# Kernel tuning notes

Measured on AMD Instinct MI355X. Metric: run time of the kernel, lower is better.

Reference implementation:

```python
import jax, jax.numpy as jnp
import numpy as np

B, N, C, H, V = 32, 1024, 512, 256, 50  # batch, positions, post_conv_out_channels, hidden_size, out_channels


def setup_inputs() -> dict:
    key = jax.random.key(0)
    ks = jax.random.split(key, 9)
    s = 0.05
    p = lambda k, shape: jax.random.normal(k, shape, jnp.float32) * s
    return dict(
        features=jax.random.normal(ks[0], (B, N, C), jnp.float32),
        w_i2h=p(ks[1], (H, C)),              # input_to_hidden (no bias)
        w_h2h=p(ks[2], (H, H)), b_h2h=jnp.zeros((H,), jnp.float32),
        w_score=p(ks[3], (H,)),              # score Linear(H,1,no bias)
        w_gru_ih=p(ks[4], (3 * H, C + V)), w_gru_hh=p(ks[5], (3 * H, H)),
        b_gru_ih=jnp.zeros((3 * H,), jnp.float32), b_gru_hh=jnp.zeros((3 * H,), jnp.float32),
        w_s1=p(ks[6], (H, H)), b_s1=jnp.zeros((H,), jnp.float32),
        w_s2=p(ks[7], (V, H)), b_s2=jnp.zeros((V,), jnp.float32),
        max_text_length=500,
    )


def reference(features, w_i2h, w_h2h, b_h2h, w_score, w_gru_ih, w_gru_hh,
              b_gru_ih, b_gru_hh, w_s1, b_s1, w_s2, b_s2, max_text_length):
    batch = features.shape[0]
    hid = w_h2h.shape[0]
    vocab = w_s2.shape[0]
    steps = max_text_length + 1
    # input_to_hidden(features) is loop-invariant -> hoist out of the recurrence
    feat_proj = jnp.einsum('bnc,hc->bnh', features, w_i2h)

    def gru_cell(x, h):
        gi = x @ w_gru_ih.T + b_gru_ih
        gh = h @ w_gru_hh.T + b_gru_hh
        i_r, i_z, i_n = jnp.split(gi, 3, axis=-1)
        h_r, h_z, h_n = jnp.split(gh, 3, axis=-1)
        r = jax.nn.sigmoid(i_r + h_r)
        z = jax.nn.sigmoid(i_z + h_z)
        n = jnp.tanh(i_n + r * h_n)
        return (1.0 - z) * n + z * h

    def step(carry, _):
        h, pre = carry
        prev_proj = h @ w_h2h.T + b_h2h                      # [B,H]
        scores = jnp.tanh(feat_proj + prev_proj[:, None, :]) @ w_score  # [B,N]
        alpha = jax.nn.softmax(scores, axis=1)
        ctx = jnp.einsum('bn,bnc->bc', alpha, features)      # [B,C]
        onehot = jax.nn.one_hot(pre, vocab, dtype=features.dtype)
        h_new = gru_cell(jnp.concatenate([ctx, onehot], axis=-1), h)
        struct = (h_new @ w_s1.T + b_s1) @ w_s2.T + b_s2     # structure_generator, [B,V]
        pre_new = jnp.argmax(struct, axis=-1)
        return (h_new, pre_new), struct

    h0 = jnp.zeros((batch, hid), features.dtype)
    pre0 = jnp.zeros((batch,), jnp.int32)
    _, structs = jax.lax.scan(step, (h0, pre0), None, length=steps)  # [T,B,V]
    structs = jnp.transpose(structs, (1, 0, 2))                      # [B,T,V]
    return jax.nn.softmax(structs, axis=-1)
```

## Files before the change

kernel.cpp:

```cpp
#include <hip/hip_runtime.h>
#include <math.h>

#define B_ 32
#define N_ 1024
#define C_ 512
#define H_ 256
#define V_ 50
#define T_ 501
#define CV_ 562
#define G3_ 768
#define CHUNKS_ 32
#define POSB_ 32

typedef float    f32x4 __attribute__((ext_vector_type(4)));
typedef _Float16 f16x4 __attribute__((ext_vector_type(4)));
typedef _Float16 f16x8 __attribute__((ext_vector_type(8)));

__device__ __forceinline__ float fast_rcp(float x) { return __builtin_amdgcn_rcpf(x); }
__device__ __forceinline__ float fast_tanh(float x) {
  float e = __expf(2.0f * x);
  return 1.0f - 2.0f * fast_rcp(e + 1.0f);
}
__device__ __forceinline__ float fast_sigmoid(float x) {
  return fast_rcp(1.0f + __expf(-x));
}
__device__ __forceinline__ void astore(float* p, float v) {
  __hip_atomic_store(p, v, __ATOMIC_RELAXED, __HIP_MEMORY_SCOPE_AGENT);
}
__device__ __forceinline__ float aload(const float* p) {
  return __hip_atomic_load(p, __ATOMIC_RELAXED, __HIP_MEMORY_SCOPE_AGENT);
}
__device__ __forceinline__ int aloadi(const int* p) {
  return __hip_atomic_load(p, __ATOMIC_RELAXED, __HIP_MEMORY_SCOPE_AGENT);
}

__global__ __launch_bounds__(256) void fp_gemm(const float* __restrict__ A,
                                               const float* __restrict__ W,
                                               _Float16* __restrict__ FPh) {
  __shared__ __align__(16) float As[16][68];
  __shared__ __align__(16) float Ws[16][68];
  const int t = threadIdx.x;
  const int m0 = blockIdx.x * 64;
  const int h0 = blockIdx.y * 64;
  const int lr = t & 63;
  const int kg = t >> 6;
  const int tx = t & 15, ty = t >> 4;
  float acc[4][4] = {};
  for (int k0 = 0; k0 < C_; k0 += 16) {
    float4 av = *(const float4*)&A[(size_t)(m0 + lr) * C_ + k0 + kg * 4];
    float4 wv = *(const float4*)&W[(size_t)(h0 + lr) * C_ + k0 + kg * 4];
    As[kg*4+0][lr] = av.x; As[kg*4+1][lr] = av.y; As[kg*4+2][lr] = av.z; As[kg*4+3][lr] = av.w;
    Ws[kg*4+0][lr] = wv.x; Ws[kg*4+1][lr] = wv.y; Ws[kg*4+2][lr] = wv.z; Ws[kg*4+3][lr] = wv.w;
    __syncthreads();
#pragma unroll
    for (int kk = 0; kk < 16; ++kk) {
      float4 a = *(const float4*)&As[kk][ty * 4];
      float4 w = *(const float4*)&Ws[kk][tx * 4];
      acc[0][0] += a.x*w.x; acc[0][1] += a.x*w.y; acc[0][2] += a.x*w.z; acc[0][3] += a.x*w.w;
      acc[1][0] += a.y*w.x; acc[1][1] += a.y*w.y; acc[1][2] += a.y*w.z; acc[1][3] += a.y*w.w;
      acc[2][0] += a.z*w.x; acc[2][1] += a.z*w.y; acc[2][2] += a.z*w.z; acc[2][3] += a.z*w.w;
      acc[3][0] += a.w*w.x; acc[3][1] += a.w*w.y; acc[3][2] += a.w*w.z; acc[3][3] += a.w*w.w;
    }
    __syncthreads();
  }
#pragma unroll
  for (int i = 0; i < 4; ++i) {
    f16x4 o;
    o.x = (_Float16)acc[i][0]; o.y = (_Float16)acc[i][1];
    o.z = (_Float16)acc[i][2]; o.w = (_Float16)acc[i][3];
    *(f16x4*)&FPh[(size_t)(m0 + ty*4 + i) * H_ + h0 + tx*4] = o;
  }
}

__global__ void feat_to_fp16(const float* __restrict__ src, _Float16* __restrict__ dst,
                             int total4) {
  int i = blockIdx.x * 256 + threadIdx.x;
  if (i >= total4) return;
  f32x4 v = *(const f32x4*)&src[(size_t)i * 4];
  f16x4 o; o.x = (_Float16)v.x; o.y = (_Float16)v.y; o.z = (_Float16)v.z; o.w = (_Float16)v.w;
  *(f16x4*)&dst[(size_t)i * 4] = o;
}

__global__ void transpose_split(const float* __restrict__ src, float* __restrict__ dstA,
                                float* __restrict__ dstB, int rows, int cols, int splitc) {
  int i = blockIdx.x * 256 + threadIdx.x;
  if (i >= rows * cols) return;
  int j = i / cols, c = i - j * cols;
  float v = src[i];
  if (c < splitc) dstA[(size_t)c * rows + j] = v;
  else            dstB[(size_t)(c - splitc) * rows + j] = v;
}

__global__ void init_kernel(const float* __restrict__ b_h2h, float* __restrict__ h,
                            float* __restrict__ pp, int* __restrict__ pre,
                            int* __restrict__ cnt1, int* __restrict__ cnt2) {
  int i = blockIdx.x * blockDim.x + threadIdx.x;
  if (i < B_ * H_) { h[i] = 0.0f; pp[i] = b_h2h[i & (H_ - 1)]; }
  if (i < B_) pre[i] = 0;
  if (i < T_ * B_ * 16) cnt1[i] = 0;
  if (i < T_ * 16) cnt2[i] = 0;
}

__global__ __launch_bounds__(256) void k1_attn(
    int tstep,
    const _Float16* __restrict__ feath, const _Float16* __restrict__ fph,
    const float* __restrict__ w_score, const float* __restrict__ pp,
    float* __restrict__ part_ctx, float* __restrict__ part_l, int* __restrict__ cnt1,
    float* __restrict__ ctx_raw, float* __restrict__ l_total) {
  __shared__ __align__(16) float lds_ctx[4 * C_];
  __shared__ float lds_l[4];
  __shared__ int sflag;

  const int t = threadIdx.x;
  const int wv = t >> 6;
  const int lane = t & 63;
  const int b = blockIdx.x >> 5;
  const int chunk = blockIdx.x & (CHUNKS_ - 1);

  float4 ppr = *(const float4*)&pp[b * H_ + lane * 4];
  float4 wsr = *(const float4*)&w_score[lane * 4];
  float aA0 = 0.f, aA1 = 0.f, aA2 = 0.f, aA3 = 0.f;
  float aB0 = 0.f, aB1 = 0.f, aB2 = 0.f, aB3 = 0.f;
  float lacc = 0.f;
  const _Float16* fphb = fph + (size_t)b * N_ * H_;
  const _Float16* fbb  = feath + (size_t)b * N_ * C_;
  const int n0 = chunk * POSB_ + wv * 8;
#pragma unroll 2
  for (int i = 0; i < 8; ++i) {
    const int n = n0 + i;
    f16x4 v = __builtin_nontemporal_load((const f16x4*)&fphb[(size_t)n * H_ + lane * 4]);
    float s = fast_tanh((float)v.x + ppr.x) * wsr.x + fast_tanh((float)v.y + ppr.y) * wsr.y
            + fast_tanh((float)v.z + ppr.z) * wsr.z + fast_tanh((float)v.w + ppr.w) * wsr.w;
#pragma unroll
    for (int off = 32; off > 0; off >>= 1) s += __shfl_xor(s, off);
    float p = __expf(s);
    lacc += p;
    f16x8 f = __builtin_nontemporal_load((const f16x8*)&fbb[(size_t)n * C_ + lane * 8]);
    aA0 += p * (float)f.s0; aA1 += p * (float)f.s1; aA2 += p * (float)f.s2; aA3 += p * (float)f.s3;
    aB0 += p * (float)f.s4; aB1 += p * (float)f.s5; aB2 += p * (float)f.s6; aB3 += p * (float)f.s7;
  }
  {
    float4 o0; o0.x = aA0; o0.y = aA1; o0.z = aA2; o0.w = aA3;
    float4 o1; o1.x = aB0; o1.y = aB1; o1.z = aB2; o1.w = aB3;
    *(float4*)&lds_ctx[wv * C_ + lane * 8] = o0;
    *(float4*)&lds_ctx[wv * C_ + lane * 8 + 4] = o1;
  }
  if (lane == 0) lds_l[wv] = lacc;
  __syncthreads();
  {
    float c0 = lds_ctx[t] + lds_ctx[C_ + t] + lds_ctx[2 * C_ + t] + lds_ctx[3 * C_ + t];
    float c1 = lds_ctx[t + 256] + lds_ctx[C_ + t + 256] + lds_ctx[2 * C_ + t + 256] + lds_ctx[3 * C_ + t + 256];
    float* pc = &part_ctx[((size_t)b * CHUNKS_ + chunk) * C_];
    astore(&pc[t], c0);
    astore(&pc[t + 256], c1);
    if (t == 0) astore(&part_l[b * CHUNKS_ + chunk], lds_l[0] + lds_l[1] + lds_l[2] + lds_l[3]);
  }
  asm volatile("s_waitcnt vmcnt(0)" ::: "memory");
  __syncthreads();
  if (t == 0) sflag = atomicAdd(&cnt1[(tstep * B_ + b) * 16], 1);
  __syncthreads();
  if (sflag != CHUNKS_ - 1) return;

  float d0 = 0.f, d1 = 0.f;
  const float* src = part_ctx + (size_t)b * CHUNKS_ * C_;
#pragma unroll 8
  for (int ch = 0; ch < CHUNKS_; ++ch) {
    d0 += aload(&src[(size_t)ch * C_ + t]);
    d1 += aload(&src[(size_t)ch * C_ + t + 256]);
  }
  ctx_raw[b * C_ + t] = d0;
  ctx_raw[b * C_ + t + 256] = d1;
  if (t < 64) {
    float lv = (t < CHUNKS_) ? aload(&part_l[b * CHUNKS_ + t]) : 0.0f;
#pragma unroll
    for (int off = 32; off > 0; off >>= 1) lv += __shfl_xor(lv, off);
    if (t == 0) l_total[b] = lv;
  }
}

__global__ __launch_bounds__(256) void k2_fused(
    int tstep,
    const float* __restrict__ ctx_raw, float* __restrict__ h,
    const float* __restrict__ WtA, const float* __restrict__ WtH,
    float* __restrict__ pgi, float* __restrict__ pgh,
    const float* __restrict__ l_total,
    const float* __restrict__ WtO,
    const float* __restrict__ b_gru_ih, const float* __restrict__ b_gru_hh,
    const float* __restrict__ Wt_s1, const float* __restrict__ b_s1,
    const float* __restrict__ Wt_h2h, const float* __restrict__ b_h2h,
    const float* __restrict__ w_s2, const float* __restrict__ b_s2,
    float* __restrict__ pp, int* __restrict__ pre,
    int* __restrict__ cnt2, float* __restrict__ out) {
  __shared__ __align__(16) float smem[6144];
  __shared__ int sflag;
  const int t = threadIdx.x;
  const int j0 = (blockIdx.x % 12) * 64;
  const int ks = blockIdx.x / 12;
  float* wlds = smem;
  float* clds = smem + 4096;
  const int jl = (t & 31) * 2;
  const int b0 = (t >> 5) * 4;

  float acc[2][4] = {};
#pragma unroll
  for (int kt = 0; kt < 2; ++kt) {
    const int k0 = ks * 128 + kt * 64;
    __syncthreads();
#pragma unroll
    for (int q = 0; q < 4; ++q) {
      int idx = q * 256 + t; int r = idx >> 4, f4 = (idx & 15) * 4;
      *(float4*)&wlds[r * 64 + f4] = *(const float4*)&WtA[(size_t)(k0 + r) * G3_ + j0 + f4];
    }
#pragma unroll
    for (int q = 0; q < 2; ++q) {
      int idx = q * 256 + t; int bb = idx >> 4, f4 = (idx & 15) * 4;
      *(float4*)&clds[bb * 64 + f4] = *(const float4*)&ctx_raw[(size_t)bb * C_ + k0 + f4];
    }
    __syncthreads();
#pragma unroll 8
    for (int k = 0; k < 64; ++k) {
      float w0 = wlds[k * 64 + jl], w1 = wlds[k * 64 + jl + 1];
      float x0 = clds[b0 * 64 + k], x1 = clds[(b0 + 1) * 64 + k];
      float x2 = clds[(b0 + 2) * 64 + k], x3 = clds[(b0 + 3) * 64 + k];
      acc[0][0] += w0 * x0; acc[0][1] += w0 * x1; acc[0][2] += w0 * x2; acc[0][3] += w0 * x3;
      acc[1][0] += w1 * x0; acc[1][1] += w1 * x1; acc[1][2] += w1 * x2; acc[1][3] += w1 * x3;
    }
  }
#pragma unroll
  for (int i = 0; i < 2; ++i)
#pragma unroll
    for (int q = 0; q < 4; ++q)
      astore(&pgi[((size_t)ks * B_ + b0 + q) * G3_ + j0 + jl + i], acc[i][q]);

  float acb[2][4] = {};
  {
    const int k0 = ks * 64;
    __syncthreads();
#pragma unroll
    for (int q = 0; q < 4; ++q) {
      int idx = q * 256 + t; int r = idx >> 4, f4 = (idx & 15) * 4;
      *(float4*)&wlds[r * 64 + f4] = *(const float4*)&WtH[(size_t)(k0 + r) * G3_ + j0 + f4];
    }
#pragma unroll
    for (int q = 0; q < 2; ++q) {
      int idx = q * 256 + t; int bb = idx >> 4, f4 = (idx & 15) * 4;
      *(float4*)&clds[bb * 64 + f4] = *(const float4*)&h[(size_t)bb * H_ + k0 + f4];
    }
    __syncthreads();
#pragma unroll 8
    for (int k = 0; k < 64; ++k) {
      float w0 = wlds[k * 64 + jl], w1 = wlds[k * 64 + jl + 1];
      float x0 = clds[b0 * 64 + k], x1 = clds[(b0 + 1) * 64 + k];
      float x2 = clds[(b0 + 2) * 64 + k], x3 = clds[(b0 + 3) * 64 + k];
      acb[0][0] += w0 * x0; acb[0][1] += w0 * x1; acb[0][2] += w0 * x2; acb[0][3] += w0 * x3;
      acb[1][0] += w1 * x0; acb[1][1] += w1 * x1; acb[1][2] += w1 * x2; acb[1][3] += w1 * x3;
    }
  }
#pragma unroll
  for (int i = 0; i < 2; ++i)
#pragma unroll
    for (int q = 0; q < 4; ++q)
      astore(&pgh[((size_t)ks * B_ + b0 + q) * G3_ + j0 + jl + i], acb[i][q]);

  asm volatile("s_waitcnt vmcnt(0)" ::: "memory");
  __syncthreads();
  if (t == 0) sflag = atomicAdd(&cnt2[tstep * 16], 1);
  __syncthreads();
  const int ticket = sflag;
  if (ticket < 16) return;
  if (t == 0) {
    while (aloadi(&cnt2[tstep * 16]) < 48) __builtin_amdgcn_s_sleep(2);
  }
  __syncthreads();

  const int b = ticket - 16;
  float* shn = smem;
  float* ss1 = smem + 256;
  float* sst = smem + 512;
  const int prev = pre[b];
  const float invl = 1.0f / l_total[b];
  float gi0 = 0.f, gi1 = 0.f, gi2 = 0.f, gh0 = 0.f, gh1 = 0.f, gh2 = 0.f;
#pragma unroll
  for (int k = 0; k < 4; ++k) {
    const float* pg = pgi + ((size_t)k * B_ + b) * G3_;
    const float* ph = pgh + ((size_t)k * B_ + b) * G3_;
    gi0 += aload(&pg[t]); gi1 += aload(&pg[t + 256]); gi2 += aload(&pg[t + 512]);
    gh0 += aload(&ph[t]); gh1 += aload(&ph[t + 256]); gh2 += aload(&ph[t + 512]);
  }
  const float* wo = WtO + (size_t)prev * G3_;
  gi0 = gi0 * invl + b_gru_ih[t]       + wo[t];
  gi1 = gi1 * invl + b_gru_ih[t + 256] + wo[t + 256];
  gi2 = gi2 * invl + b_gru_ih[t + 512] + wo[t + 512];
  gh0 += b_gru_hh[t]; gh1 += b_gru_hh[t + 256]; gh2 += b_gru_hh[t + 512];
  const float h_old = h[b * H_ + t];
  const float r = fast_sigmoid(gi0 + gh0);
  const float z = fast_sigmoid(gi1 + gh1);
  const float nn = fast_tanh(gi2 + r * gh2);
  const float hnew = (1.0f - z) * nn + z * h_old;
  h[b * H_ + t] = hnew;
  shn[t] = hnew;
  __syncthreads();

  {
    float a1 = b_s1[t], a2 = b_h2h[t];
    const float* w1 = Wt_s1 + t;
    const float* w2 = Wt_h2h + t;
#pragma unroll 8
    for (int c = 0; c < H_; ++c) {
      float v = shn[c];
      a1 += w1[(size_t)c * H_] * v;
      a2 += w2[(size_t)c * H_] * v;
    }
    ss1[t] = a1;
    pp[b * H_ + t] = a2;
  }
  __syncthreads();

  const int wv = t >> 6, lane = t & 63;
  for (int v = wv; v < V_; v += 4) {
    float4 wr = *(const float4*)&w_s2[(size_t)v * H_ + lane * 4];
    float4 sv = *(const float4*)&ss1[lane * 4];
    float acc2 = wr.x * sv.x + wr.y * sv.y + wr.z * sv.z + wr.w * sv.w;
#pragma unroll
    for (int off = 32; off > 0; off >>= 1) acc2 += __shfl_xor(acc2, off);
    if (lane == 0) sst[v] = acc2 + b_s2[v];
  }
  __syncthreads();

  if (t < 64) {
    float val = (lane < V_) ? sst[lane] : -INFINITY;
    float m = val;
#pragma unroll
    for (int off = 32; off > 0; off >>= 1) m = fmaxf(m, __shfl_xor(m, off));
    unsigned long long msk = __ballot(val == m);
    int amax = __ffsll(msk) - 1;
    float e = (lane < V_) ? __expf(val - m) : 0.0f;
    float ssum = e;
#pragma unroll
    for (int off = 32; off > 0; off >>= 1) ssum += __shfl_xor(ssum, off);
    if (lane < V_) out[((size_t)b * T_ + tstep) * V_ + lane] = e / ssum;
    if (lane == 0) pre[b] = amax;
  }
}

extern "C" void kernel_launch(void* const* d_in, const int* in_sizes, int n_in,
                              void* d_out, int out_size, void* d_ws, size_t ws_size,
                              hipStream_t stream) {
  (void)in_sizes; (void)n_in; (void)out_size; (void)ws_size;
  const float* feat     = (const float*)d_in[0];
  const float* w_i2h    = (const float*)d_in[1];
  const float* w_h2h    = (const float*)d_in[2];
  const float* b_h2h    = (const float*)d_in[3];
  const float* w_score  = (const float*)d_in[4];
  const float* w_gru_ih = (const float*)d_in[5];
  const float* w_gru_hh = (const float*)d_in[6];
  const float* b_gru_ih = (const float*)d_in[7];
  const float* b_gru_hh = (const float*)d_in[8];
  const float* w_s1     = (const float*)d_in[9];
  const float* b_s1     = (const float*)d_in[10];
  const float* w_s2     = (const float*)d_in[11];
  const float* b_s2     = (const float*)d_in[12];
  float* out = (float*)d_out;

  char* ws = (char*)d_ws;
  size_t off = 0;
  auto alloc = [&](size_t bytes) { void* p = ws + off; off += (bytes + 255) & ~(size_t)255; return p; };
  _Float16* fph   = (_Float16*)alloc((size_t)B_ * N_ * H_ * 2);
  _Float16* feath = (_Float16*)alloc((size_t)B_ * N_ * C_ * 2);
  float* part_ctx = (float*)alloc((size_t)B_ * CHUNKS_ * C_ * 4);
  float* part_l   = (float*)alloc((size_t)B_ * CHUNKS_ * 4);
  float* ctx_raw  = (float*)alloc((size_t)B_ * C_ * 4);
  float* l_total  = (float*)alloc((size_t)B_ * 4);
  float* pgi      = (float*)alloc((size_t)4 * B_ * G3_ * 4);
  float* pgh      = (float*)alloc((size_t)4 * B_ * G3_ * 4);
  float* WtA      = (float*)alloc((size_t)C_ * G3_ * 4);
  float* WtO      = (float*)alloc((size_t)V_ * G3_ * 4);
  float* WtH      = (float*)alloc((size_t)H_ * G3_ * 4);
  float* Wt_s1    = (float*)alloc((size_t)H_ * H_ * 4);
  float* Wt_h2h   = (float*)alloc((size_t)H_ * H_ * 4);
  float* h        = (float*)alloc((size_t)B_ * H_ * 4);
  float* pp       = (float*)alloc((size_t)B_ * H_ * 4);
  int*   pre      = (int*)alloc((size_t)B_ * 4);
  int*   cnt1     = (int*)alloc((size_t)T_ * B_ * 16 * 4);
  int*   cnt2     = (int*)alloc((size_t)T_ * 16 * 4);

  init_kernel<<<(T_ * B_ * 16 + 255) / 256, 256, 0, stream>>>(b_h2h, h, pp, pre, cnt1, cnt2);
  fp_gemm<<<dim3((B_ * N_) / 64, H_ / 64), 256, 0, stream>>>(feat, w_i2h, fph);
  feat_to_fp16<<<(B_ * N_ * C_ / 4 + 255) / 256, 256, 0, stream>>>(feat, feath, B_ * N_ * C_ / 4);
  transpose_split<<<(G3_ * CV_ + 255) / 256, 256, 0, stream>>>(w_gru_ih, WtA, WtO, G3_, CV_, C_);
  transpose_split<<<(G3_ * H_ + 255) / 256, 256, 0, stream>>>(w_gru_hh, WtH, WtH, G3_, H_, H_);
  transpose_split<<<(H_ * H_ + 255) / 256, 256, 0, stream>>>(w_s1, Wt_s1, Wt_s1, H_, H_, H_);
  transpose_split<<<(H_ * H_ + 255) / 256, 256, 0, stream>>>(w_h2h, Wt_h2h, Wt_h2h, H_, H_, H_);

  for (int tstep = 0; tstep < T_; ++tstep) {
    k1_attn<<<B_ * CHUNKS_, 256, 0, stream>>>(tstep, feath, fph, w_score, pp,
                                              part_ctx, part_l, cnt1, ctx_raw, l_total);
    k2_fused<<<48, 256, 0, stream>>>(tstep, ctx_raw, h, WtA, WtH, pgi, pgh, l_total,
                                     WtO, b_gru_ih, b_gru_hh, Wt_s1, b_s1, Wt_h2h, b_h2h,
                                     w_s2, b_s2, pp, pre, cnt2, out);
  }
}
```

Measured before the change: 18.11 ms.

## Move chunk reduction from attention kernel into tail kernel with grid barriers

The attention kernel no longer does the last-block atomic ticket and the cross-chunk reduction. It just writes partial context sums, and it now issues all eight position loads up front so more memory requests are in flight. The tail kernel's first 32 blocks reduce the partials per batch, then all 48 blocks pass a spin barrier before the GRU gate GEMM. A second barrier replaces the ticket-based election of the 32 GRU finisher blocks. This shortens the attention kernel's critical path, at the cost of an extra grid-wide spin barrier inside the tail kernel and more registers in the attention kernel.

```diff
diff --git a/kernel.cpp b/kernel.cpp
--- a/kernel.cpp
+++ b/kernel.cpp
@@ -93,23 +93,19 @@
 
 __global__ void init_kernel(const float* __restrict__ b_h2h, float* __restrict__ h,
                             float* __restrict__ pp, int* __restrict__ pre,
-                            int* __restrict__ cnt1, int* __restrict__ cnt2) {
+                            int* __restrict__ cnt) {
   int i = blockIdx.x * blockDim.x + threadIdx.x;
   if (i < B_ * H_) { h[i] = 0.0f; pp[i] = b_h2h[i & (H_ - 1)]; }
   if (i < B_) pre[i] = 0;
-  if (i < T_ * B_ * 16) cnt1[i] = 0;
-  if (i < T_ * 16) cnt2[i] = 0;
+  if (i < T_ * 16) cnt[i] = 0;
 }
 
 __global__ __launch_bounds__(256) void k1_attn(
-    int tstep,
     const _Float16* __restrict__ feath, const _Float16* __restrict__ fph,
     const float* __restrict__ w_score, const float* __restrict__ pp,
-    float* __restrict__ part_ctx, float* __restrict__ part_l, int* __restrict__ cnt1,
-    float* __restrict__ ctx_raw, float* __restrict__ l_total) {
+    float* __restrict__ part_ctx, float* __restrict__ part_l) {
   __shared__ __align__(16) float lds_ctx[4 * C_];
   __shared__ float lds_l[4];
-  __shared__ int sflag;
 
   const int t = threadIdx.x;
   const int wv = t >> 6;
@@ -119,25 +115,31 @@
 
   float4 ppr = *(const float4*)&pp[b * H_ + lane * 4];
   float4 wsr = *(const float4*)&w_score[lane * 4];
+  const int n0 = chunk * POSB_ + wv * 8;
+  const _Float16* fp0 = fph + (size_t)b * N_ * H_ + (size_t)n0 * H_ + lane * 4;
+  const _Float16* ft0 = feath + (size_t)b * N_ * C_ + (size_t)n0 * C_ + lane * 8;
+
+  f16x4 v[8];
+  f16x8 f[8];
+#pragma unroll
+  for (int i = 0; i < 8; ++i) {
+    v[i] = __builtin_nontemporal_load((const f16x4*)(fp0 + (size_t)i * H_));
+    f[i] = __builtin_nontemporal_load((const f16x8*)(ft0 + (size_t)i * C_));
+  }
+
   float aA0 = 0.f, aA1 = 0.f, aA2 = 0.f, aA3 = 0.f;
   float aB0 = 0.f, aB1 = 0.f, aB2 = 0.f, aB3 = 0.f;
   float lacc = 0.f;
-  const _Float16* fphb = fph + (size_t)b * N_ * H_;
-  const _Float16* fbb  = feath + (size_t)b * N_ * C_;
-  const int n0 = chunk * POSB_ + wv * 8;
-#pragma unroll 2
+#pragma unroll
   for (int i = 0; i < 8; ++i) {
-    const int n = n0 + i;
-    f16x4 v = __builtin_nontemporal_load((const f16x4*)&fphb[(size_t)n * H_ + lane * 4]);
-    float s = fast_tanh((float)v.x + ppr.x) * wsr.x + fast_tanh((float)v.y + ppr.y) * wsr.y
-            + fast_tanh((float)v.z + ppr.z) * wsr.z + fast_tanh((float)v.w + ppr.w) * wsr.w;
+    float s = fast_tanh((float)v[i].x + ppr.x) * wsr.x + fast_tanh((float)v[i].y + ppr.y) * wsr.y
+            + fast_tanh((float)v[i].z + ppr.z) * wsr.z + fast_tanh((float)v[i].w + ppr.w) * wsr.w;
 #pragma unroll
     for (int off = 32; off > 0; off >>= 1) s += __shfl_xor(s, off);
     float p = __expf(s);
     lacc += p;
-    f16x8 f = __builtin_nontemporal_load((const f16x8*)&fbb[(size_t)n * C_ + lane * 8]);
-    aA0 += p * (float)f.s0; aA1 += p * (float)f.s1; aA2 += p * (float)f.s2; aA3 += p * (float)f.s3;
-    aB0 += p * (float)f.s4; aB1 += p * (float)f.s5; aB2 += p * (float)f.s6; aB3 += p * (float)f.s7;
+    aA0 += p * (float)f[i].s0; aA1 += p * (float)f[i].s1; aA2 += p * (float)f[i].s2; aA3 += p * (float)f[i].s3;
+    aB0 += p * (float)f[i].s4; aB1 += p * (float)f[i].s5; aB2 += p * (float)f[i].s6; aB3 += p * (float)f[i].s7;
   }
   {
     float4 o0; o0.x = aA0; o0.y = aA1; o0.z = aA2; o0.w = aA3;
@@ -151,195 +153,203 @@
     float c0 = lds_ctx[t] + lds_ctx[C_ + t] + lds_ctx[2 * C_ + t] + lds_ctx[3 * C_ + t];
     float c1 = lds_ctx[t + 256] + lds_ctx[C_ + t + 256] + lds_ctx[2 * C_ + t + 256] + lds_ctx[3 * C_ + t + 256];
     float* pc = &part_ctx[((size_t)b * CHUNKS_ + chunk) * C_];
-    astore(&pc[t], c0);
-    astore(&pc[t + 256], c1);
-    if (t == 0) astore(&part_l[b * CHUNKS_ + chunk], lds_l[0] + lds_l[1] + lds_l[2] + lds_l[3]);
-  }
-  asm volatile("s_waitcnt vmcnt(0)" ::: "memory");
-  __syncthreads();
-  if (t == 0) sflag = atomicAdd(&cnt1[(tstep * B_ + b) * 16], 1);
-  __syncthreads();
-  if (sflag != CHUNKS_ - 1) return;
-
-  float d0 = 0.f, d1 = 0.f;
-  const float* src = part_ctx + (size_t)b * CHUNKS_ * C_;
-#pragma unroll 8
-  for (int ch = 0; ch < CHUNKS_; ++ch) {
-    d0 += aload(&src[(size_t)ch * C_ + t]);
-    d1 += aload(&src[(size_t)ch * C_ + t + 256]);
-  }
-  ctx_raw[b * C_ + t] = d0;
-  ctx_raw[b * C_ + t + 256] = d1;
-  if (t < 64) {
-    float lv = (t < CHUNKS_) ? aload(&part_l[b * CHUNKS_ + t]) : 0.0f;
-#pragma unroll
-    for (int off = 32; off > 0; off >>= 1) lv += __shfl_xor(lv, off);
-    if (t == 0) l_total[b] = lv;
-  }
-}
-
-__global__ __launch_bounds__(256) void k2_fused(
+    pc[t] = c0;
+    pc[t + 256] = c1;
+    if (t == 0) part_l[b * CHUNKS_ + chunk] = lds_l[0] + lds_l[1] + lds_l[2] + lds_l[3];
+  }
+}
+
+__global__ __launch_bounds__(256) void ktail(
     int tstep,
-    const float* __restrict__ ctx_raw, float* __restrict__ h,
+    const float* __restrict__ part_ctx, const float* __restrict__ part_l,
+    float* __restrict__ ctx_raw, float* __restrict__ l_total,
+    float* __restrict__ h,
     const float* __restrict__ WtA, const float* __restrict__ WtH,
     float* __restrict__ pgi, float* __restrict__ pgh,
-    const float* __restrict__ l_total,
     const float* __restrict__ WtO,
     const float* __restrict__ b_gru_ih, const float* __restrict__ b_gru_hh,
     const float* __restrict__ Wt_s1, const float* __restrict__ b_s1,
     const float* __restrict__ Wt_h2h, const float* __restrict__ b_h2h,
     const float* __restrict__ w_s2, const float* __restrict__ b_s2,
     float* __restrict__ pp, int* __restrict__ pre,
-    int* __restrict__ cnt2, float* __restrict__ out) {
+    int* __restrict__ cnt, float* __restrict__ out) {
   __shared__ __align__(16) float smem[6144];
-  __shared__ int sflag;
+  const int blk = blockIdx.x;
   const int t = threadIdx.x;
-  const int j0 = (blockIdx.x % 12) * 64;
-  const int ks = blockIdx.x / 12;
-  float* wlds = smem;
-  float* clds = smem + 4096;
-  const int jl = (t & 31) * 2;
-  const int b0 = (t >> 5) * 4;
-
-  float acc[2][4] = {};
-#pragma unroll
-  for (int kt = 0; kt < 2; ++kt) {
-    const int k0 = ks * 128 + kt * 64;
-    __syncthreads();
-#pragma unroll
-    for (int q = 0; q < 4; ++q) {
-      int idx = q * 256 + t; int r = idx >> 4, f4 = (idx & 15) * 4;
-      *(float4*)&wlds[r * 64 + f4] = *(const float4*)&WtA[(size_t)(k0 + r) * G3_ + j0 + f4];
-    }
-#pragma unroll
-    for (int q = 0; q < 2; ++q) {
-      int idx = q * 256 + t; int bb = idx >> 4, f4 = (idx & 15) * 4;
-      *(float4*)&clds[bb * 64 + f4] = *(const float4*)&ctx_raw[(size_t)bb * C_ + k0 + f4];
-    }
-    __syncthreads();
+
+  if (blk < B_) {
+    const int b = blk;
+    const float* src = part_ctx + (size_t)b * CHUNKS_ * C_;
+    float s0 = 0.f, s1 = 0.f;
 #pragma unroll 8
-    for (int k = 0; k < 64; ++k) {
-      float w0 = wlds[k * 64 + jl], w1 = wlds[k * 64 + jl + 1];
-      float x0 = clds[b0 * 64 + k], x1 = clds[(b0 + 1) * 64 + k];
-      float x2 = clds[(b0 + 2) * 64 + k], x3 = clds[(b0 + 3) * 64 + k];
-      acc[0][0] += w0 * x0; acc[0][1] += w0 * x1; acc[0][2] += w0 * x2; acc[0][3] += w0 * x3;
-      acc[1][0] += w1 * x0; acc[1][1] += w1 * x1; acc[1][2] += w1 * x2; acc[1][3] += w1 * x3;
-    }
-  }
-#pragma unroll
-  for (int i = 0; i < 2; ++i)
-#pragma unroll
-    for (int q = 0; q < 4; ++q)
-      astore(&pgi[((size_t)ks * B_ + b0 + q) * G3_ + j0 + jl + i], acc[i][q]);
-
-  float acb[2][4] = {};
-  {
-    const int k0 = ks * 64;
-    __syncthreads();
-#pragma unroll
-    for (int q = 0; q < 4; ++q) {
-      int idx = q * 256 + t; int r = idx >> 4, f4 = (idx & 15) * 4;
-      *(float4*)&wlds[r * 64 + f4] = *(const float4*)&WtH[(size_t)(k0 + r) * G3_ + j0 + f4];
-    }
-#pragma unroll
-    for (int q = 0; q < 2; ++q) {
-      int idx = q * 256 + t; int bb = idx >> 4, f4 = (idx & 15) * 4;
-      *(float4*)&clds[bb * 64 + f4] = *(const float4*)&h[(size_t)bb * H_ + k0 + f4];
-    }
-    __syncthreads();
-#pragma unroll 8
-    for (int k = 0; k < 64; ++k) {
-      float w0 = wlds[k * 64 + jl], w1 = wlds[k * 64 + jl + 1];
-      float x0 = clds[b0 * 64 + k], x1 = clds[(b0 + 1) * 64 + k];
-      float x2 = clds[(b0 + 2) * 64 + k], x3 = clds[(b0 + 3) * 64 + k];
-      acb[0][0] += w0 * x0; acb[0][1] += w0 * x1; acb[0][2] += w0 * x2; acb[0][3] += w0 * x3;
-      acb[1][0] += w1 * x0; acb[1][1] += w1 * x1; acb[1][2] += w1 * x2; acb[1][3] += w1 * x3;
-    }
-  }
-#pragma unroll
-  for (int i = 0; i < 2; ++i)
-#pragma unroll
-    for (int q = 0; q < 4; ++q)
-      astore(&pgh[((size_t)ks * B_ + b0 + q) * G3_ + j0 + jl + i], acb[i][q]);
-
+    for (int ch = 0; ch < CHUNKS_; ++ch) {
+      s0 += src[(size_t)ch * C_ + t];
+      s1 += src[(size_t)ch * C_ + t + 256];
+    }
+    astore(&ctx_raw[b * C_ + t], s0);
+    astore(&ctx_raw[b * C_ + t + 256], s1);
+    if (t < 64) {
+      float lv = (t < CHUNKS_) ? part_l[b * CHUNKS_ + t] : 0.0f;
+#pragma unroll
+      for (int off = 32; off > 0; off >>= 1) lv += __shfl_xor(lv, off);
+      if (t == 0) astore(&l_total[b], lv);
+    }
+  }
   asm volatile("s_waitcnt vmcnt(0)" ::: "memory");
   __syncthreads();
-  if (t == 0) sflag = atomicAdd(&cnt2[tstep * 16], 1);
+  if (t == 0) {
+    atomicAdd(&cnt[tstep * 16], 1);
+    while (aloadi(&cnt[tstep * 16]) < 48) __builtin_amdgcn_s_sleep(1);
+  }
   __syncthreads();
-  const int ticket = sflag;
-  if (ticket < 16) return;
+
+  {
+    const int jg = blk % 12, ks = blk / 12;
+    const int j0 = jg * 64;
+    const int jl = (t & 31) * 2;
+    const int b0 = (t >> 5) * 4;
+    float* wlds = smem;
+    float* clds = smem + 4096;
+
+    float acc[2][4] = {};
+#pragma unroll
+    for (int kt = 0; kt < 2; ++kt) {
+      const int k0 = ks * 128 + kt * 64;
+      __syncthreads();
+#pragma unroll
+      for (int q = 0; q < 4; ++q) {
+        int idx = q * 256 + t; int r = idx >> 4, f4 = (idx & 15) * 4;
+        *(float4*)&wlds[r * 64 + f4] = *(const float4*)&WtA[(size_t)(k0 + r) * G3_ + j0 + f4];
+      }
+#pragma unroll
+      for (int q = 0; q < 8; ++q) {
+        int idx = q * 256 + t; int bb = idx >> 6, k = idx & 63;
+        clds[bb * 64 + k] = aload(&ctx_raw[bb * C_ + k0 + k]);
+      }
+      __syncthreads();
+#pragma unroll 8
+      for (int k = 0; k < 64; ++k) {
+        float w0 = wlds[k * 64 + jl], w1 = wlds[k * 64 + jl + 1];
+        float x0 = clds[b0 * 64 + k], x1 = clds[(b0 + 1) * 64 + k];
+        float x2 = clds[(b0 + 2) * 64 + k], x3 = clds[(b0 + 3) * 64 + k];
+        acc[0][0] += w0 * x0; acc[0][1] += w0 * x1; acc[0][2] += w0 * x2; acc[0][3] += w0 * x3;
+        acc[1][0] += w1 * x0; acc[1][1] += w1 * x1; acc[1][2] += w1 * x2; acc[1][3] += w1 * x3;
+      }
+    }
+#pragma unroll
+    for (int i = 0; i < 2; ++i)
+#pragma unroll
+      for (int q = 0; q < 4; ++q)
+        astore(&pgi[((size_t)ks * B_ + b0 + q) * G3_ + j0 + jl + i], acc[i][q]);
+
+    float acb[2][4] = {};
+    {
+      const int k0 = ks * 64;
+      __syncthreads();
+#pragma unroll
+      for (int q = 0; q < 4; ++q) {
+        int idx = q * 256 + t; int r = idx >> 4, f4 = (idx & 15) * 4;
+        *(float4*)&wlds[r * 64 + f4] = *(const float4*)&WtH[(size_t)(k0 + r) * G3_ + j0 + f4];
+      }
+#pragma unroll
+      for (int q = 0; q < 2; ++q) {
+        int idx = q * 256 + t; int bb = idx >> 4, f4 = (idx & 15) * 4;
+        *(float4*)&clds[bb * 64 + f4] = *(const float4*)&h[(size_t)bb * H_ + k0 + f4];
+      }
+      __syncthreads();
+#pragma unroll 8
+      for (int k = 0; k < 64; ++k) {
+        float w0 = wlds[k * 64 + jl], w1 = wlds[k * 64 + jl + 1];
+        float x0 = clds[b0 * 64 + k], x1 = clds[(b0 + 1) * 64 + k];
+        float x2 = clds[(b0 + 2) * 64 + k], x3 = clds[(b0 + 3) * 64 + k];
+        acb[0][0] += w0 * x0; acb[0][1] += w0 * x1; acb[0][2] += w0 * x2; acb[0][3] += w0 * x3;
+        acb[1][0] += w1 * x0; acb[1][1] += w1 * x1; acb[1][2] += w1 * x2; acb[1][3] += w1 * x3;
+      }
+    }
+#pragma unroll
+    for (int i = 0; i < 2; ++i)
+#pragma unroll
+      for (int q = 0; q < 4; ++q)
+        astore(&pgh[((size_t)ks * B_ + b0 + q) * G3_ + j0 + jl + i], acb[i][q]);
+  }
+  asm volatile("s_waitcnt vmcnt(0)" ::: "memory");
+  __syncthreads();
+  if (t == 0) atomicAdd(&cnt[tstep * 16 + 8], 1);
+  if (blk >= B_) return;
   if (t == 0) {
-    while (aloadi(&cnt2[tstep * 16]) < 48) __builtin_amdgcn_s_sleep(2);
+    while (aloadi(&cnt[tstep * 16 + 8]) < 48) __builtin_amdgcn_s_sleep(1);
   }
   __syncthreads();
 
-  const int b = ticket - 16;
-  float* shn = smem;
-  float* ss1 = smem + 256;
-  float* sst = smem + 512;
-  const int prev = pre[b];
-  const float invl = 1.0f / l_total[b];
-  float gi0 = 0.f, gi1 = 0.f, gi2 = 0.f, gh0 = 0.f, gh1 = 0.f, gh2 = 0.f;
-#pragma unroll
-  for (int k = 0; k < 4; ++k) {
-    const float* pg = pgi + ((size_t)k * B_ + b) * G3_;
-    const float* ph = pgh + ((size_t)k * B_ + b) * G3_;
-    gi0 += aload(&pg[t]); gi1 += aload(&pg[t + 256]); gi2 += aload(&pg[t + 512]);
-    gh0 += aload(&ph[t]); gh1 += aload(&ph[t + 256]); gh2 += aload(&ph[t + 512]);
-  }
-  const float* wo = WtO + (size_t)prev * G3_;
-  gi0 = gi0 * invl + b_gru_ih[t]       + wo[t];
-  gi1 = gi1 * invl + b_gru_ih[t + 256] + wo[t + 256];
-  gi2 = gi2 * invl + b_gru_ih[t + 512] + wo[t + 512];
-  gh0 += b_gru_hh[t]; gh1 += b_gru_hh[t + 256]; gh2 += b_gru_hh[t + 512];
-  const float h_old = h[b * H_ + t];
-  const float r = fast_sigmoid(gi0 + gh0);
-  const float z = fast_sigmoid(gi1 + gh1);
-  const float nn = fast_tanh(gi2 + r * gh2);
-  const float hnew = (1.0f - z) * nn + z * h_old;
-  h[b * H_ + t] = hnew;
-  shn[t] = hnew;
-  __syncthreads();
-
   {
-    float a1 = b_s1[t], a2 = b_h2h[t];
-    const float* w1 = Wt_s1 + t;
-    const float* w2 = Wt_h2h + t;
+    const int b = blk;
+    float* shn = smem;
+    float* ss1 = smem + 256;
+    float* sst = smem + 512;
+    const int prev = pre[b];
+    const float invl = 1.0f / aload(&l_total[b]);
+    float gi0 = 0.f, gi1 = 0.f, gi2 = 0.f, gh0 = 0.f, gh1 = 0.f, gh2 = 0.f;
+#pragma unroll
+    for (int ks = 0; ks < 4; ++ks) {
+      const float* pg = pgi + ((size_t)ks * B_ + b) * G3_;
+      const float* ph = pgh + ((size_t)ks * B_ + b) * G3_;
+      gi0 += aload(&pg[t]); gi1 += aload(&pg[t + 256]); gi2 += aload(&pg[t + 512]);
+      gh0 += aload(&ph[t]); gh1 += aload(&ph[t + 256]); gh2 += aload(&ph[t + 512]);
+    }
+    const float* wo = WtO + (size_t)prev * G3_;
+    gi0 = gi0 * invl + b_gru_ih[t]       + wo[t];
+    gi1 = gi1 * invl + b_gru_ih[t + 256] + wo[t + 256];
+    gi2 = gi2 * invl + b_gru_ih[t + 512] + wo[t + 512];
+    gh0 += b_gru_hh[t]; gh1 += b_gru_hh[t + 256]; gh2 += b_gru_hh[t + 512];
+    const float h_old = h[b * H_ + t];
+    const float r = fast_sigmoid(gi0 + gh0);
+    const float z = fast_sigmoid(gi1 + gh1);
+    const float nn = fast_tanh(gi2 + r * gh2);
+    const float hnew = (1.0f - z) * nn + z * h_old;
+    h[b * H_ + t] = hnew;
+    shn[t] = hnew;
+    __syncthreads();
+
+    {
+      float a1 = b_s1[t], a2 = b_h2h[t];
+      const float* w1 = Wt_s1 + t;
+      const float* w2 = Wt_h2h + t;
 #pragma unroll 8
-    for (int c = 0; c < H_; ++c) {
-      float v = shn[c];
-      a1 += w1[(size_t)c * H_] * v;
-      a2 += w2[(size_t)c * H_] * v;
-    }
-    ss1[t] = a1;
-    pp[b * H_ + t] = a2;
-  }
-  __syncthreads();
-
-  const int wv = t >> 6, lane = t & 63;
-  for (int v = wv; v < V_; v += 4) {
-    float4 wr = *(const float4*)&w_s2[(size_t)v * H_ + lane * 4];
-    float4 sv = *(const float4*)&ss1[lane * 4];
-    float acc2 = wr.x * sv.x + wr.y * sv.y + wr.z * sv.z + wr.w * sv.w;
-#pragma unroll
-    for (int off = 32; off > 0; off >>= 1) acc2 += __shfl_xor(acc2, off);
-    if (lane == 0) sst[v] = acc2 + b_s2[v];
-  }
-  __syncthreads();
-
-  if (t < 64) {
-    float val = (lane < V_) ? sst[lane] : -INFINITY;
-    float m = val;
-#pragma unroll
-    for (int off = 32; off > 0; off >>= 1) m = fmaxf(m, __shfl_xor(m, off));
-    unsigned long long msk = __ballot(val == m);
-    int amax = __ffsll(msk) - 1;
-    float e = (lane < V_) ? __expf(val - m) : 0.0f;
-    float ssum = e;
-#pragma unroll
-    for (int off = 32; off > 0; off >>= 1) ssum += __shfl_xor(ssum, off);
-    if (lane < V_) out[((size_t)b * T_ + tstep) * V_ + lane] = e / ssum;
-    if (lane == 0) pre[b] = amax;
+      for (int c = 0; c < H_; ++c) {
+        float vv = shn[c];
+        a1 += w1[(size_t)c * H_] * vv;
+        a2 += w2[(size_t)c * H_] * vv;
+      }
+      ss1[t] = a1;
+      pp[b * H_ + t] = a2;
+    }
+    __syncthreads();
+
+    const int wv = t >> 6, lane = t & 63;
+    for (int vv = wv; vv < V_; vv += 4) {
+      float4 wr = *(const float4*)&w_s2[(size_t)vv * H_ + lane * 4];
+      float4 sv = *(const float4*)&ss1[lane * 4];
+      float acc = wr.x * sv.x + wr.y * sv.y + wr.z * sv.z + wr.w * sv.w;
+#pragma unroll
+      for (int off = 32; off > 0; off >>= 1) acc += __shfl_xor(acc, off);
+      if (lane == 0) sst[vv] = acc + b_s2[vv];
+    }
+    __syncthreads();
+
+    if (t < 64) {
+      float val = (lane < V_) ? sst[lane] : -INFINITY;
+      float m = val;
+#pragma unroll
+      for (int off = 32; off > 0; off >>= 1) m = fmaxf(m, __shfl_xor(m, off));
+      unsigned long long msk = __ballot(val == m);
+      int amax = __ffsll(msk) - 1;
+      float e = (lane < V_) ? __expf(val - m) : 0.0f;
+      float ssum = e;
+#pragma unroll
+      for (int off = 32; off > 0; off >>= 1) ssum += __shfl_xor(ssum, off);
+      if (lane < V_) out[((size_t)b * T_ + tstep) * V_ + lane] = e / ssum;
+      if (lane == 0) pre[b] = amax;
+    }
   }
 }
 
@@ -381,10 +391,9 @@
   float* h        = (float*)alloc((size_t)B_ * H_ * 4);
   float* pp       = (float*)alloc((size_t)B_ * H_ * 4);
   int*   pre      = (int*)alloc((size_t)B_ * 4);
-  int*   cnt1     = (int*)alloc((size_t)T_ * B_ * 16 * 4);
-  int*   cnt2     = (int*)alloc((size_t)T_ * 16 * 4);
-
-  init_kernel<<<(T_ * B_ * 16 + 255) / 256, 256, 0, stream>>>(b_h2h, h, pp, pre, cnt1, cnt2);
+  int*   cnt      = (int*)alloc((size_t)T_ * 16 * 4);
+
+  init_kernel<<<(T_ * 16 + 255) / 256, 256, 0, stream>>>(b_h2h, h, pp, pre, cnt);
   fp_gemm<<<dim3((B_ * N_) / 64, H_ / 64), 256, 0, stream>>>(feat, w_i2h, fph);
   feat_to_fp16<<<(B_ * N_ * C_ / 4 + 255) / 256, 256, 0, stream>>>(feat, feath, B_ * N_ * C_ / 4);
   transpose_split<<<(G3_ * CV_ + 255) / 256, 256, 0, stream>>>(w_gru_ih, WtA, WtO, G3_, CV_, C_);
@@ -393,10 +402,10 @@
   transpose_split<<<(H_ * H_ + 255) / 256, 256, 0, stream>>>(w_h2h, Wt_h2h, Wt_h2h, H_, H_, H_);
 
   for (int tstep = 0; tstep < T_; ++tstep) {
-    k1_attn<<<B_ * CHUNKS_, 256, 0, stream>>>(tstep, feath, fph, w_score, pp,
-                                              part_ctx, part_l, cnt1, ctx_raw, l_total);
-    k2_fused<<<48, 256, 0, stream>>>(tstep, ctx_raw, h, WtA, WtH, pgi, pgh, l_total,
-                                     WtO, b_gru_ih, b_gru_hh, Wt_s1, b_s1, Wt_h2h, b_h2h,
-                                     w_s2, b_s2, pp, pre, cnt2, out);
-  }
-}
+    k1_attn<<<B_ * CHUNKS_, 256, 0, stream>>>(feath, fph, w_score, pp, part_ctx, part_l);
+    ktail<<<48, 256, 0, stream>>>(tstep, part_ctx, part_l, ctx_raw, l_total, h,
+                                  WtA, WtH, pgi, pgh, WtO,
+                                  b_gru_ih, b_gru_hh, Wt_s1, b_s1, Wt_h2h, b_h2h,
+                                  w_s2, b_s2, pp, pre, cnt, out);
+  }
+}
```

After: 20.20 ms. +11.5%, slower.
